# Optimization experiments

Measured on AMD Instinct MI355X. Metric: run time of the kernel, lower is better.

The kernel has to match this reference:

```python
import jax, jax.numpy as jnp
import numpy as np

B, S, D, H = 2, 4096, 768, 12
HD = D // H
SCALE = HD ** -0.5


def setup_inputs() -> dict:
    key = jax.random.key(0)
    k_x, k_wq, k_bq, k_wp, k_bp = jax.random.split(key, 5)
    lim_qkv = (1.0 / D) ** 0.5
    lim_p = (1.0 / D) ** 0.5
    return {
        "x": jax.random.normal(k_x, (B, S, D), dtype=jnp.float32),
        "qkv_w": jax.random.uniform(k_wq, (3 * D, D), dtype=jnp.float32, minval=-lim_qkv, maxval=lim_qkv),
        "qkv_b": jax.random.uniform(k_bq, (3 * D,), dtype=jnp.float32, minval=-lim_qkv, maxval=lim_qkv),
        "proj_w": jax.random.uniform(k_wp, (D, D), dtype=jnp.float32, minval=-lim_p, maxval=lim_p),
        "proj_b": jax.random.uniform(k_bp, (D,), dtype=jnp.float32, minval=-lim_p, maxval=lim_p),
    }


def reference(x, qkv_w, qkv_b, proj_w, proj_b):
    b, s, _ = x.shape
    qkv = x @ qkv_w.T + qkv_b                      # [b, s, 3D]
    q, k, v = jnp.split(qkv, 3, axis=-1)           # each [b, s, D]
    # [b, s, D] -> [b, H, s, HD]
    def to_heads(t):
        return t.reshape(b, s, H, HD).transpose(0, 2, 1, 3)
    q, k, v = to_heads(q), to_heads(k), to_heads(v)
    attn = jnp.einsum("bhqd,bhkd->bhqk", q, k) * SCALE   # [b, H, s, s]
    attn = jax.nn.softmax(attn, axis=-1)
    out = jnp.einsum("bhqk,bhkd->bhqd", attn, v)         # [b, H, s, HD]
    out = out.transpose(0, 2, 1, 3).reshape(b, s, D)
    return out @ proj_w.T + proj_b
```

## Files before the change

kernel.cpp:

```cpp
#include <hip/hip_runtime.h>
#include <hip/hip_bf16.h>


#define B_ 2
#define S_ 4096
#define D_ 768
#define H_ 12
#define HD_ 64
#define TD_ (3 * D_)
#define QKD_ (2 * D_)

static constexpr float LOG2E = 1.4426950408889634f;
static constexpr float QSCL = 0.125f * LOG2E;

typedef __bf16 bf16x8 __attribute__((ext_vector_type(8)));
typedef unsigned short ushortx8 __attribute__((ext_vector_type(8)));
typedef unsigned short ushortx4 __attribute__((ext_vector_type(4)));
typedef float floatx4 __attribute__((ext_vector_type(4)));

__device__ inline unsigned short f2bf(float f) {
  return __builtin_bit_cast(unsigned short, (__bf16)f);
}
__device__ inline float bf2f(unsigned short u) {
  return __uint_as_float(((unsigned int)u) << 16);
}
__device__ inline void glds16(const unsigned short* g, unsigned short* l) {
  __builtin_amdgcn_global_load_lds(
      (const __attribute__((address_space(1))) unsigned int*)g,
      (__attribute__((address_space(3))) unsigned int*)l, 16, 0, 0);
}

__global__ __launch_bounds__(256)
void cvt_all(const float* __restrict__ s0, unsigned short* __restrict__ d0, int n0,
             const float* __restrict__ s1, unsigned short* __restrict__ d1, int n1,
             const float* __restrict__ s2, unsigned short* __restrict__ d2, int n2) {
  int idx = blockIdx.x * 256 + threadIdx.x;
  const float* s; unsigned short* d;
  if (idx < n0) { s = s0; d = d0; }
  else if (idx < n0 + n1) { s = s1; d = d1; idx -= n0; }
  else if (idx < n0 + n1 + n2) { s = s2; d = d2; idx -= n0 + n1; }
  else return;
  floatx4 v = *reinterpret_cast<const floatx4*>(&s[(size_t)idx * 4]);
  ushortx4 o;
#pragma unroll
  for (int j = 0; j < 4; ++j) o[j] = f2bf(v[j]);
  *reinterpret_cast<ushortx4*>(&d[(size_t)idx * 4]) = o;
}

template <int NFR, bool QKV_EPI>
__global__ __launch_bounds__(256)
void gemm_bf16(const unsigned short* __restrict__ A,
               const unsigned short* __restrict__ W,
               const float* __restrict__ bias,
               float* __restrict__ Cf,
               unsigned short* __restrict__ qkbuf,
               unsigned short* __restrict__ vT,
               int M, int N, int K) {
  constexpr int BM = 128, BN = NFR * 32, BK = 64;
  __shared__ __attribute__((aligned(16))) unsigned short As[BM][BK];
  __shared__ __attribute__((aligned(16))) unsigned short Ws[BN][BK];

  const int tid = threadIdx.x;
  const int lane = tid & 63;
  const int wid = tid >> 6;
  const int wm = wid >> 1;
  const int wn = wid & 1;
  const int m0 = blockIdx.y * BM;
  const int n0 = blockIdx.x * BN;
  const int lr = lane & 15;
  const int g = lane >> 4;
  const int e8 = lr & 7;
  const int ro = g * 4;
  const int srow = lane >> 3;
  const int sch = lane & 7;

  floatx4 acc[4][NFR];
#pragma unroll
  for (int m = 0; m < 4; ++m)
#pragma unroll
    for (int n = 0; n < NFR; ++n) acc[m][n] = (floatx4){0.f, 0.f, 0.f, 0.f};

  for (int kb = 0; kb < K; kb += BK) {
#pragma unroll
    for (int c = 0; c < 4; ++c) {
      int seg = wid * 4 + c;
      int row = seg * 8 + srow;
      glds16(&A[(size_t)(m0 + row) * K + kb + ((sch ^ srow) << 3)], &As[seg * 8][0]);
    }
#pragma unroll
    for (int c = 0; c < NFR; ++c) {
      int seg = wid * NFR + c;
      int row = seg * 8 + srow;
      glds16(&W[(size_t)(n0 + row) * K + kb + ((sch ^ srow) << 3)], &Ws[seg * 8][0]);
    }
    __syncthreads();

#pragma unroll
    for (int ks = 0; ks < 2; ++ks) {
      int ch = ((ks << 2) + g) ^ e8;
      bf16x8 af[4], bfr[NFR];
#pragma unroll
      for (int m = 0; m < 4; ++m)
        af[m] = *reinterpret_cast<const bf16x8*>(&As[wm * 64 + m * 16 + lr][ch << 3]);
#pragma unroll
      for (int n = 0; n < NFR; ++n)
        bfr[n] = *reinterpret_cast<const bf16x8*>(&Ws[wn * (NFR * 16) + n * 16 + lr][ch << 3]);
#pragma unroll
      for (int m = 0; m < 4; ++m)
#pragma unroll
        for (int n = 0; n < NFR; ++n)
          acc[m][n] = __builtin_amdgcn_mfma_f32_16x16x32_bf16(af[m], bfr[n], acc[m][n], 0, 0, 0);
    }
    __syncthreads();
  }

#pragma unroll
  for (int n = 0; n < NFR; ++n) {
    int col = n0 + wn * (NFR * 16) + n * 16 + lr;
    float bv = bias[col];
#pragma unroll
    for (int m = 0; m < 4; ++m) {
      int row = m0 + wm * 64 + m * 16 + ro;
      if constexpr (QKV_EPI) {
        if (col >= QKD_) {
          int dcol = col - QKD_;
          int hh = dcol >> 6, dd = dcol & 63;
          int bb = row >> 12, s = row & (S_ - 1);
          int s5 = s & 31;
          int spos = (s & ~31) + ((s5 >> 2) & 3) * 8 + ((s5 >> 4) & 1) * 4;
          ushortx4 o4;
#pragma unroll
          for (int i = 0; i < 4; ++i) o4[i] = f2bf(acc[m][n][i] + bv);
          *reinterpret_cast<ushortx4*>(
              &vT[(size_t)((bb * H_ + hh) * 64 + dd) * S_ + spos]) = o4;
        } else {
          const float scl = (col < D_) ? QSCL : 1.0f;
#pragma unroll
          for (int i = 0; i < 4; ++i)
            qkbuf[(size_t)(row + i) * QKD_ + col] = f2bf((acc[m][n][i] + bv) * scl);
        }
      } else {
#pragma unroll
        for (int i = 0; i < 4; ++i)
          Cf[(size_t)(row + i) * N + col] = acc[m][n][i] + bv;
      }
    }
  }
}

__global__ __launch_bounds__(256)
void attn_kernel(const unsigned short* __restrict__ qkbuf,
                 const unsigned short* __restrict__ vT,
                 unsigned short* __restrict__ outb) {
  constexpr int QB = 128, KVB = 64, NT = S_ / KVB;
  __shared__ __attribute__((aligned(16))) unsigned short L[2 * 8192];

  const int tid = threadIdx.x;
  const int lane = tid & 63;
  const int wid = tid >> 6;
  const int q0 = blockIdx.x * QB;
  const int h = blockIdx.y;
  const int b = blockIdx.z;
  const int lr = lane & 15;
  const int g = lane >> 4;
  const int e8 = lr & 7;
  const int wq = wid * 32;

  const unsigned short* Qg = qkbuf + (size_t)b * S_ * QKD_ + (size_t)h * HD_;
  const unsigned short* Kg = Qg + D_;
  const unsigned short* Vg = vT + (size_t)(b * H_ + h) * HD_ * S_;

  const int srow = lane >> 3;
  const int sch = lane & 7;

  bf16x8 qf[2][2];
#pragma unroll
  for (int qt = 0; qt < 2; ++qt)
#pragma unroll
    for (int ks = 0; ks < 2; ++ks)
      qf[qt][ks] = *reinterpret_cast<const bf16x8*>(
          &Qg[(size_t)(q0 + wq + qt * 16 + lr) * QKD_ + ks * 32 + g * 8]);

  bf16x8 onesf;
#pragma unroll
  for (int j = 0; j < 8; ++j) onesf[j] = (__bf16)1.0f;

  floatx4 lacc[2] = {(floatx4){0.f, 0.f, 0.f, 0.f}, (floatx4){0.f, 0.f, 0.f, 0.f}};
  floatx4 oacc[2][4];
#pragma unroll
  for (int qt = 0; qt < 2; ++qt)
#pragma unroll
    for (int dt = 0; dt < 4; ++dt) oacc[qt][dt] = (floatx4){0.f, 0.f, 0.f, 0.f};

  int koff[4][2], voff[2][4];
#pragma unroll
  for (int kt = 0; kt < 4; ++kt)
#pragma unroll
    for (int ks = 0; ks < 2; ++ks)
      koff[kt][ks] = (kt * 16 + lr) * 64 + ((((ks << 2) + g) ^ e8) << 3);
#pragma unroll
  for (int ks = 0; ks < 2; ++ks)
#pragma unroll
    for (int dt = 0; dt < 4; ++dt)
      voff[ks][dt] = 4096 + (dt * 16 + lr) * 64 + ((((ks << 2) + g) ^ e8) << 3);

  const unsigned short* kp0 = Kg + (size_t)(wid * 16 + srow) * QKD_ + ((sch ^ srow) << 3);
  const unsigned short* kp1 = kp0 + (size_t)8 * QKD_;
  const unsigned short* vp0 = Vg + (size_t)(wid * 16 + srow) * S_ + ((sch ^ srow) << 3);
  const unsigned short* vp1 = vp0 + (size_t)8 * S_;

#define STAGE(BUF) do { \
    glds16(kp0, &L[(BUF) * 8192 + (wid * 16) * 64]); \
    glds16(kp1, &L[(BUF) * 8192 + (wid * 16 + 8) * 64]); \
    glds16(vp0, &L[(BUF) * 8192 + 4096 + (wid * 16) * 64]); \
    glds16(vp1, &L[(BUF) * 8192 + 4096 + (wid * 16 + 8) * 64]); \
    kp0 += (size_t)KVB * QKD_; kp1 += (size_t)KVB * QKD_; \
    vp0 += KVB; vp1 += KVB; } while (0)

#define COMPUTE(BUF) do { \
    bf16x8 kf[4][2], vf[2][4]; \
    _Pragma("unroll") \
    for (int kt = 0; kt < 4; ++kt) \
      _Pragma("unroll") \
      for (int ks = 0; ks < 2; ++ks) \
        kf[kt][ks] = *reinterpret_cast<const bf16x8*>(&L[(BUF) * 8192 + koff[kt][ks]]); \
    _Pragma("unroll") \
    for (int ks = 0; ks < 2; ++ks) \
      _Pragma("unroll") \
      for (int dt = 0; dt < 4; ++dt) \
        vf[ks][dt] = *reinterpret_cast<const bf16x8*>(&L[(BUF) * 8192 + voff[ks][dt]]); \
    _Pragma("unroll") \
    for (int qt = 0; qt < 2; ++qt) { \
      floatx4 sc[4]; \
      _Pragma("unroll") \
      for (int kt = 0; kt < 4; ++kt) { \
        floatx4 c = (floatx4){0.f, 0.f, 0.f, 0.f}; \
        _Pragma("unroll") \
        for (int ks = 0; ks < 2; ++ks) \
          c = __builtin_amdgcn_mfma_f32_16x16x32_bf16(kf[kt][ks], qf[qt][ks], c, 0, 0, 0); \
        sc[kt] = c; \
      } \
      _Pragma("unroll") \
      for (int kt = 0; kt < 4; ++kt) \
        _Pragma("unroll") \
        for (int i = 0; i < 4; ++i) \
          sc[kt][i] = __builtin_amdgcn_exp2f(sc[kt][i]); \
      bf16x8 pf0, pf1; \
      _Pragma("unroll") \
      for (int j = 0; j < 8; ++j) { \
        pf0[j] = (__bf16)sc[(j >> 2)][j & 3]; \
        pf1[j] = (__bf16)sc[2 + (j >> 2)][j & 3]; \
      } \
      lacc[qt] = __builtin_amdgcn_mfma_f32_16x16x32_bf16(onesf, pf0, lacc[qt], 0, 0, 0); \
      lacc[qt] = __builtin_amdgcn_mfma_f32_16x16x32_bf16(onesf, pf1, lacc[qt], 0, 0, 0); \
      _Pragma("unroll") \
      for (int dt = 0; dt < 4; ++dt) \
        oacc[qt][dt] = __builtin_amdgcn_mfma_f32_16x16x32_bf16(vf[0][dt], pf0, oacc[qt][dt], 0, 0, 0); \
      _Pragma("unroll") \
      for (int dt = 0; dt < 4; ++dt) \
        oacc[qt][dt] = __builtin_amdgcn_mfma_f32_16x16x32_bf16(vf[1][dt], pf1, oacc[qt][dt], 0, 0, 0); \
    } } while (0)

  STAGE(0);
  for (int t = 0; t < NT; t += 2) {
    __syncthreads();
    STAGE(1);
    COMPUTE(0);
    __syncthreads();
    if (t + 2 < NT) STAGE(0);
    COMPUTE(1);
  }
#undef STAGE
#undef COMPUTE

#pragma unroll
  for (int qt = 0; qt < 2; ++qt) {
    float l = lacc[qt][0];
    int q = q0 + wq + qt * 16 + lr;
    float inv = __builtin_amdgcn_rcpf(l);
    size_t rowbase = ((size_t)b * S_ + q) * D_ + h * HD_;
#pragma unroll
    for (int dt = 0; dt < 4; ++dt) {
      ushortx4 o4;
#pragma unroll
      for (int i = 0; i < 4; ++i) o4[i] = f2bf(oacc[qt][dt][i] * inv);
      *reinterpret_cast<ushortx4*>(&outb[rowbase + dt * 16 + 4 * g]) = o4;
    }
  }
}

extern "C" void kernel_launch(void* const* d_in, const int* in_sizes, int n_in,
                              void* d_out, int out_size, void* d_ws, size_t ws_size,
                              hipStream_t stream) {
  const float* x      = (const float*)d_in[0];
  const float* qkv_w  = (const float*)d_in[1];
  const float* qkv_b  = (const float*)d_in[2];
  const float* proj_w = (const float*)d_in[3];
  const float* proj_b = (const float*)d_in[4];
  float* out = (float*)d_out;

  unsigned short* qkbuf   = (unsigned short*)d_ws;
  unsigned short* vTbuf   = qkbuf + (size_t)B_ * S_ * QKD_;
  unsigned short* attnbuf = vTbuf + (size_t)B_ * H_ * HD_ * S_;
  unsigned short* xbf     = attnbuf + (size_t)B_ * S_ * D_;
  unsigned short* wqkvbf  = xbf + (size_t)B_ * S_ * D_;
  unsigned short* wprojbf = wqkvbf + (size_t)TD_ * D_;

  dim3 blk(256);
  const int nx = B_ * S_ * D_ / 4, nw1 = TD_ * D_ / 4, nw2 = D_ * D_ / 4;
  cvt_all<<<dim3((nx + nw1 + nw2 + 255) / 256), blk, 0, stream>>>(
      x, xbf, nx, qkv_w, wqkvbf, nw1, proj_w, wprojbf, nw2);

  gemm_bf16<4, true><<<dim3(TD_ / 128, (B_ * S_) / 128), blk, 0, stream>>>(
      xbf, wqkvbf, qkv_b, nullptr, qkbuf, vTbuf, B_ * S_, TD_, D_);

  attn_kernel<<<dim3(S_ / 128, H_, B_), blk, 0, stream>>>(qkbuf, vTbuf, attnbuf);

  gemm_bf16<2, false><<<dim3(D_ / 64, (B_ * S_) / 128), blk, 0, stream>>>(
      attnbuf, wprojbf, proj_b, out, nullptr, nullptr, B_ * S_, D_, D_);
}
```

Measured before the change: 187.5 us.

## Use two waves per attention block with four query tiles each

The attention kernel now runs with 128 threads (2 waves) instead of 256. Each wave handles 64 query rows (four 16-row tiles) instead of 32, and each wave stages twice as many K/V rows into shared memory. This halves the number of LDS reads of K/V fragments per query row, so register-held K/V fragments are reused across more query tiles. The cost is higher register pressure from the larger accumulator set and fewer waves per block to hide latency.

```diff
diff --git a/kernel.cpp b/kernel.cpp
--- a/kernel.cpp
+++ b/kernel.cpp
@@ -148,11 +148,11 @@
   }
 }
 
-__global__ __launch_bounds__(256)
+__global__ __launch_bounds__(128, 2)
 void attn_kernel(const unsigned short* __restrict__ qkbuf,
                  const unsigned short* __restrict__ vT,
                  unsigned short* __restrict__ outb) {
-  constexpr int QB = 128, KVB = 64, NT = S_ / KVB;
+  constexpr int QB = 128, KVB = 64, NQT = 4, NT = S_ / KVB;
   __shared__ __attribute__((aligned(16))) unsigned short L[2 * 8192];
 
   const int tid = threadIdx.x;
@@ -164,7 +164,7 @@
   const int lr = lane & 15;
   const int g = lane >> 4;
   const int e8 = lr & 7;
-  const int wq = wid * 32;
+  const int wq = wid * (NQT * 16);
 
   const unsigned short* Qg = qkbuf + (size_t)b * S_ * QKD_ + (size_t)h * HD_;
   const unsigned short* Kg = Qg + D_;
@@ -173,9 +173,9 @@
   const int srow = lane >> 3;
   const int sch = lane & 7;
 
-  bf16x8 qf[2][2];
-#pragma unroll
-  for (int qt = 0; qt < 2; ++qt)
+  bf16x8 qf[NQT][2];
+#pragma unroll
+  for (int qt = 0; qt < NQT; ++qt)
 #pragma unroll
     for (int ks = 0; ks < 2; ++ks)
       qf[qt][ks] = *reinterpret_cast<const bf16x8*>(
@@ -185,12 +185,14 @@
 #pragma unroll
   for (int j = 0; j < 8; ++j) onesf[j] = (__bf16)1.0f;
 
-  floatx4 lacc[2] = {(floatx4){0.f, 0.f, 0.f, 0.f}, (floatx4){0.f, 0.f, 0.f, 0.f}};
-  floatx4 oacc[2][4];
-#pragma unroll
-  for (int qt = 0; qt < 2; ++qt)
+  floatx4 lacc[NQT];
+  floatx4 oacc[NQT][4];
+#pragma unroll
+  for (int qt = 0; qt < NQT; ++qt) {
+    lacc[qt] = (floatx4){0.f, 0.f, 0.f, 0.f};
 #pragma unroll
     for (int dt = 0; dt < 4; ++dt) oacc[qt][dt] = (floatx4){0.f, 0.f, 0.f, 0.f};
+  }
 
   int koff[4][2], voff[2][4];
 #pragma unroll
@@ -204,18 +206,22 @@
     for (int dt = 0; dt < 4; ++dt)
       voff[ks][dt] = 4096 + (dt * 16 + lr) * 64 + ((((ks << 2) + g) ^ e8) << 3);
 
-  const unsigned short* kp0 = Kg + (size_t)(wid * 16 + srow) * QKD_ + ((sch ^ srow) << 3);
-  const unsigned short* kp1 = kp0 + (size_t)8 * QKD_;
-  const unsigned short* vp0 = Vg + (size_t)(wid * 16 + srow) * S_ + ((sch ^ srow) << 3);
-  const unsigned short* vp1 = vp0 + (size_t)8 * S_;
+  const unsigned short* kp[4];
+  const unsigned short* vp[4];
+#pragma unroll
+  for (int c = 0; c < 4; ++c) {
+    kp[c] = Kg + (size_t)(wid * 32 + c * 8 + srow) * QKD_ + ((sch ^ srow) << 3);
+    vp[c] = Vg + (size_t)(wid * 32 + c * 8 + srow) * S_ + ((sch ^ srow) << 3);
+  }
 
 #define STAGE(BUF) do { \
-    glds16(kp0, &L[(BUF) * 8192 + (wid * 16) * 64]); \
-    glds16(kp1, &L[(BUF) * 8192 + (wid * 16 + 8) * 64]); \
-    glds16(vp0, &L[(BUF) * 8192 + 4096 + (wid * 16) * 64]); \
-    glds16(vp1, &L[(BUF) * 8192 + 4096 + (wid * 16 + 8) * 64]); \
-    kp0 += (size_t)KVB * QKD_; kp1 += (size_t)KVB * QKD_; \
-    vp0 += KVB; vp1 += KVB; } while (0)
+    _Pragma("unroll") \
+    for (int c = 0; c < 4; ++c) { \
+      glds16(kp[c], &L[(BUF) * 8192 + (wid * 32 + c * 8) * 64]); \
+      glds16(vp[c], &L[(BUF) * 8192 + 4096 + (wid * 32 + c * 8) * 64]); \
+      kp[c] += (size_t)KVB * QKD_; \
+      vp[c] += KVB; \
+    } } while (0)
 
 #define COMPUTE(BUF) do { \
     bf16x8 kf[4][2], vf[2][4]; \
@@ -230,7 +236,7 @@
       for (int dt = 0; dt < 4; ++dt) \
         vf[ks][dt] = *reinterpret_cast<const bf16x8*>(&L[(BUF) * 8192 + voff[ks][dt]]); \
     _Pragma("unroll") \
-    for (int qt = 0; qt < 2; ++qt) { \
+    for (int qt = 0; qt < NQT; ++qt) { \
       floatx4 sc[4]; \
       _Pragma("unroll") \
       for (int kt = 0; kt < 4; ++kt) { \
@@ -274,7 +280,7 @@
 #undef COMPUTE
 
 #pragma unroll
-  for (int qt = 0; qt < 2; ++qt) {
+  for (int qt = 0; qt < NQT; ++qt) {
     float l = lacc[qt][0];
     int q = q0 + wq + qt * 16 + lr;
     float inv = __builtin_amdgcn_rcpf(l);
@@ -314,7 +320,7 @@
   gemm_bf16<4, true><<<dim3(TD_ / 128, (B_ * S_) / 128), blk, 0, stream>>>(
       xbf, wqkvbf, qkv_b, nullptr, qkbuf, vTbuf, B_ * S_, TD_, D_);
 
-  attn_kernel<<<dim3(S_ / 128, H_, B_), blk, 0, stream>>>(qkbuf, vTbuf, attnbuf);
+  attn_kernel<<<dim3(S_ / 128, H_, B_), dim3(128), 0, stream>>>(qkbuf, vTbuf, attnbuf);
 
   gemm_bf16<2, false><<<dim3(D_ / 64, (B_ * S_) / 128), blk, 0, stream>>>(
       attnbuf, wprojbf, proj_b, out, nullptr, nullptr, B_ * S_, D_, D_);
```

New measurement: 189.1 us. No clear change (+0.9%).
